# Kernel tuning notes

Hardware: AMD Instinct MI355X
Metric: run time of the kernel (lower is better)

Reference implementation:

```python
import jax, jax.numpy as jnp
import numpy as np

NQ, NT, BSZ, E, NH = 100, 197, 128, 768, 12
HD = E // NH
EPS = 1e-12  # torch F.normalize default eps


def _l2norm(x, axis=-1):
    n = jnp.linalg.norm(x, axis=axis, keepdims=True)
    return x / jnp.maximum(n, EPS)


def setup_inputs() -> dict:
    rng = jax.random.key(0)
    ks = jax.random.split(rng, 10)
    s = 0.02  # xavier-ish scale for weights
    return {
        "query": jax.random.normal(ks[0], (NQ, BSZ, E), jnp.float32),
        "key": jax.random.normal(ks[1], (NT, BSZ, E), jnp.float32),
        "value": jax.random.normal(ks[2], (NT, BSZ, E), jnp.float32),
        "in_proj_weight": jax.random.normal(ks[3], (3 * E, E), jnp.float32) * s,
        "in_proj_bias": jnp.zeros((3 * E,), jnp.float32),
        "out_proj_weight": jax.random.normal(ks[4], (E, E), jnp.float32) * s,
        "out_proj_bias": jnp.zeros((E,), jnp.float32),
        "temperature": jnp.ones((NH, 1, 1), jnp.float32),
        "q_mapper": jax.random.normal(ks[5], (1, NT, NQ), jnp.float32),
        "x_mapper": jax.random.normal(ks[6], (1, NQ, NT), jnp.float32),
    }


def reference(query, key, value, in_proj_weight, in_proj_bias,
              out_proj_weight, out_proj_bias, temperature, q_mapper, x_mapper):
    nq, bsz, e = query.shape
    nt = key.shape[0]
    # packed in-projection: split into q/k/v weights
    wq, wk, wv = jnp.split(in_proj_weight, 3, axis=0)
    bq, bk, bv = jnp.split(in_proj_bias, 3, axis=0)
    q = query @ wq.T + bq   # [Nq, bsz, E]
    k = key @ wk.T + bk     # [Nt, bsz, E]
    v = value @ wv.T + bv   # [Nt, bsz, E]
    # reshape to [bsz, nh, hd, N] (channel-major for cross-covariance attn)
    q = q.reshape(nq, bsz, NH, HD).transpose(1, 2, 3, 0)  # [b, h, d, Nq]
    k = k.reshape(nt, bsz, NH, HD).transpose(1, 2, 3, 0)  # [b, h, d, Nt]
    v = v.reshape(nt, bsz, NH, HD).transpose(1, 2, 3, 0)  # [b, h, d, Nt]
    # normalize channel vectors over tokens
    qn = _l2norm(q)
    kn = _l2norm(k)
    # mappers: normalize over last dim, then shape to [Nq, Nt] operators
    qm_op = _l2norm(q_mapper[0])  # [Nt, Nq] normalized over Nq; transpose below
    xm_op = _l2norm(x_mapper[0])  # [Nq, Nt] normalized over Nt
    # qm = q @ q_mapper^T : [b,h,d,Nq] x [Nq,Nt] -> [b,h,d,Nt]
    qm = jnp.einsum('bhdq,tq->bhdt', qn, qm_op)
    # cross-covariance attention over channels: [b,h,d,d]
    attn = jnp.einsum('bhdt,bhet->bhde', qm, kn) * temperature[None]  # temp [nh,1,1] broadcasts per-head
    attn = jax.nn.softmax(attn, axis=-1)
    x = jnp.einsum('bhde,bhet->bhdt', attn, v)        # [b,h,d,Nt]
    out = jnp.einsum('bhdt,qt->bhdq', x, xm_op)       # [b,h,d,Nq]
    # back to [Nq, bsz, E]
    out = out.transpose(3, 0, 1, 2).reshape(nq, bsz, e)
    out = out @ out_proj_weight.T + out_proj_bias
    return out
```

## Files before the change

kernel.cpp:

```cpp
#include <hip/hip_runtime.h>
#include <hip/hip_bf16.h>

using bf16 = __hip_bfloat16;

constexpr int NQ  = 100;
constexpr int NT  = 197;
constexpr int BSZ = 128;
constexpr int EMB = 768;
constexpr int NHD = 12;
constexpr int HDD = 64;
constexpr int COLS = BSZ * EMB;
constexpr int M_Q  = 12800;
constexpr int M_KV = 25216;
constexpr int M_KVP = 25344;
constexpr int TPAD = 224;

constexpr size_t SZ_Q16  = (size_t)M_Q  * EMB * 2;
constexpr size_t SZ_KV16 = (size_t)M_KV * EMB * 2;
constexpr size_t SZ_KVP  = (size_t)M_KVP * EMB * 2;
constexpr size_t SZ_WI   = (size_t)3 * EMB * EMB * 2;
constexpr size_t SZ_T16  = (size_t)COLS * TPAD * 2;
constexpr size_t OFF_QB   = 256;
constexpr size_t OFF_KB   = OFF_QB + SZ_Q16;
constexpr size_t OFF_VB   = OFF_KB + SZ_KV16;
constexpr size_t OFF_WI   = OFF_VB + SZ_KV16;
constexpr size_t OFF_QP16 = OFF_WI + SZ_WI;
constexpr size_t OFF_KP16 = OFF_QP16 + SZ_Q16;
constexpr size_t OFF_VP16 = OFF_KP16 + SZ_KVP;
constexpr size_t OFF_QMNT = OFF_VP16 + SZ_KVP;
constexpr size_t OFF_XMNT = OFF_QMNT + 57344;
constexpr size_t OFF_WO   = OFF_XMNT + 57344;
constexpr size_t OFF_KPT  = 256;
constexpr size_t OFF_VPT  = OFF_KPT + SZ_T16;
constexpr size_t OFF_W16T = OFF_VPT + SZ_T16;
constexpr size_t OFF_QNT  = OFF_KP16;
constexpr size_t OFF_G16  = OFF_VP16;
constexpr size_t OFF_XO   = 256;

__device__ __forceinline__ float dl(const float* p) { return *p; }
__device__ __forceinline__ float dl(const bf16* p) { return __bfloat162float(*p); }

__device__ __forceinline__ ushort f2bf(float x) {
    union { float f; unsigned u; } v; v.f = x;
    unsigned r = v.u + 0x7FFFu + ((v.u >> 16) & 1u);
    return (ushort)(r >> 16);
}
__device__ __forceinline__ float bf2f(ushort x) {
    union { unsigned u; float f; } v; v.u = (unsigned)x << 16;
    return v.f;
}
__device__ __forceinline__ void dstore(float* p, float v) { *p = v; }
__device__ __forceinline__ void dstore(bf16* p, float v) { *p = __float2bfloat16(v); }

typedef __attribute__((ext_vector_type(8))) short short8;
typedef __attribute__((ext_vector_type(4))) short shortv4;
typedef __attribute__((ext_vector_type(4))) float f32x4;

__device__ __forceinline__ void gload16(const bf16* g, ushort* l) {
    __builtin_amdgcn_global_load_lds(
        (const __attribute__((address_space(1))) unsigned int*)g,
        (__attribute__((address_space(3))) unsigned int*)l, 16, 0, 0);
}

__device__ __forceinline__ int2 xcd_swz(int bx, int by, int gx, int gy) {
    const int nwg = gx * gy;
    const int L = by * gx + bx;
    const int q = nwg >> 3, r = nwg & 7;
    const int c = L & 7, i = L >> 3;
    const int wg = (c < r ? c * (q + 1) : r * (q + 1) + (c - r) * q) + i;
    return make_int2(wg % gx, wg / gx);
}

template <typename TM>
__global__ __launch_bounds__(256) void k_cvt5(
        const float* __restrict__ s0, bf16* __restrict__ d0,
        const float* __restrict__ s1, bf16* __restrict__ d1,
        const float* __restrict__ s2, bf16* __restrict__ d2,
        const float* __restrict__ s3, bf16* __restrict__ d3,
        const float* __restrict__ s4, bf16* __restrict__ d4,
        const TM* __restrict__ qm, bf16* __restrict__ qmnT,
        const TM* __restrict__ xm, bf16* __restrict__ xmnT) {
    int bk = blockIdx.x;
    const int tid = threadIdx.x;
    if (bk >= 24864) {
        __shared__ float red[256];
        if (bk < 25088) {
            int t = bk - 24864;
            float v = (t < NT && tid < NQ) ? dl(&qm[t * NQ + tid]) : 0.f;
            if (tid < 128) red[tid] = v * v;
            __syncthreads();
            for (int s = 64; s > 0; s >>= 1) { if (tid < s) red[tid] += red[tid + s]; __syncthreads(); }
            float inv = 1.f / fmaxf(sqrtf(red[0]), 1e-12f);
            if (tid < 128)
                dstore(&qmnT[(size_t)tid * TPAD + t], (t < NT && tid < NQ) ? v * inv : 0.f);
        } else {
            int q = bk - 25088, t = tid;
            float v = (q < NQ && t < NT) ? dl(&xm[q * NT + t]) : 0.f;
            red[t] = v * v;
            __syncthreads();
            for (int s = 128; s > 0; s >>= 1) { if (t < s) red[t] += red[t + s]; __syncthreads(); }
            float inv = 1.f / fmaxf(sqrtf(red[0]), 1e-12f);
            if (t < TPAD) dstore(&xmnT[(size_t)q * TPAD + t], (q < NQ && t < NT) ? v * inv : 0.f);
        }
        return;
    }
    const float* s; bf16* d; int lb;
    if      (bk < 864)   { s = s0; d = d0; lb = bk; }
    else if (bk < 5664)  { s = s1; d = d1; lb = bk - 864; }
    else if (bk < 15120) { s = s2; d = d2; lb = bk - 5664; }
    else if (bk < 24576) { s = s3; d = d3; lb = bk - 15120; }
    else                 { s = s4; d = d4; lb = bk - 24576; }
    size_t i = ((size_t)lb * 256 + tid) * 8;
    float4 a = *(const float4*)(s + i), b = *(const float4*)(s + i + 4);
    short8 r;
    r[0] = (short)f2bf(a.x); r[1] = (short)f2bf(a.y); r[2] = (short)f2bf(a.z); r[3] = (short)f2bf(a.w);
    r[4] = (short)f2bf(b.x); r[5] = (short)f2bf(b.y); r[6] = (short)f2bf(b.z); r[7] = (short)f2bf(b.w);
    *(short8*)(d + i) = r;
}

template <typename T>
__global__ __launch_bounds__(256) void k_maps(const T* __restrict__ qm, bf16* qmnT,
                                              const T* __restrict__ xm, bf16* xmnT) {
    __shared__ float red[256];
    const int bk = blockIdx.x, tid = threadIdx.x;
    if (bk < 224) {
        int t = bk;
        float v = (t < NT && tid < NQ) ? dl(&qm[t * NQ + tid]) : 0.f;
        if (tid < 128) red[tid] = v * v;
        __syncthreads();
        for (int s = 64; s > 0; s >>= 1) { if (tid < s) red[tid] += red[tid + s]; __syncthreads(); }
        float inv = 1.f / fmaxf(sqrtf(red[0]), 1e-12f);
        if (tid < 128)
            dstore(&qmnT[(size_t)tid * TPAD + t], (t < NT && tid < NQ) ? v * inv : 0.f);
    } else {
        int q = bk - 224, t = tid;
        float v = (q < NQ && t < NT) ? dl(&xm[q * NT + t]) : 0.f;
        red[t] = v * v;
        __syncthreads();
        for (int s = 128; s > 0; s >>= 1) { if (t < s) red[t] += red[t + s]; __syncthreads(); }
        float inv = 1.f / fmaxf(sqrtf(red[0]), 1e-12f);
        if (t < TPAD) dstore(&xmnT[(size_t)q * TPAD + t], (q < NQ && t < NT) ? v * inv : 0.f);
    }
}

template <int NR, int TP, int NORM>
__global__ __launch_bounds__(256) void k_trn(const bf16* __restrict__ src,
        bf16* __restrict__ dst) {
    __shared__ ushort tile[TP * 73];
    __shared__ float ssp[4][64];
    __shared__ float inv_s[64];
    const int col0 = blockIdx.x * 64;
    const int tid = threadIdx.x;
    const int c = tid & 63, tb = tid >> 6;
    float ss = 0.f;
#pragma unroll
    for (int it = 0; it < TP / 4; ++it) {
        int t = tb + it * 4;
        ushort v = 0;
        if (t < NR) v = *(const ushort*)&src[(size_t)t * COLS + col0 + c];
        tile[t * 73 + c] = v;
        if (NORM) { float f = bf2f(v); ss = fmaf(f, f, ss); }
    }
    if (NORM) {
        ssp[tb][c] = ss;
        __syncthreads();
        if (tid < 64) {
            float s = ssp[0][tid] + ssp[1][tid] + ssp[2][tid] + ssp[3][tid];
            inv_s[tid] = 1.f / fmaxf(sqrtf(s), 1e-12f);
        }
    }
    __syncthreads();
    constexpr int UPC = TP / 8;
#pragma unroll
    for (int it = 0; it < (64 * UPC) / 256; ++it) {
        int u = tid + it * 256;
        int cc = u / UPC, t0 = (u % UPC) * 8;
        float inv = NORM ? inv_s[cc] : 1.f;
        short8 s;
#pragma unroll
        for (int r = 0; r < 8; ++r) {
            ushort raw = tile[(t0 + r) * 73 + cc];
            s[r] = NORM ? (short)f2bf(bf2f(raw) * inv) : (short)raw;
        }
        *(short8*)&dst[(size_t)(col0 + cc) * TP + t0] = s;
    }
}

__global__ __launch_bounds__(256) void k_trn2(const bf16* __restrict__ kp,
        const bf16* __restrict__ vp, bf16* __restrict__ kpT, bf16* __restrict__ vpT) {
    __shared__ ushort tile[TPAD * 73];
    __shared__ float ssp[4][64];
    __shared__ float inv_s[64];
    const int bk = blockIdx.x;
    const bool vseg = bk >= 1536;
    const bf16* src = vseg ? vp : kp;
    bf16* dst = vseg ? vpT : kpT;
    const int col0 = (vseg ? bk - 1536 : bk) * 64;
    const int tid = threadIdx.x;
    const int c = tid & 63, tb = tid >> 6;
    float ss = 0.f;
#pragma unroll
    for (int it = 0; it < TPAD / 4; ++it) {
        int t = tb + it * 4;
        ushort v = 0;
        if (t < NT) v = *(const ushort*)&src[(size_t)t * COLS + col0 + c];
        tile[t * 73 + c] = v;
        if (!vseg) { float f = bf2f(v); ss = fmaf(f, f, ss); }
    }
    if (!vseg) {
        ssp[tb][c] = ss;
        __syncthreads();
        if (tid < 64) {
            float s = ssp[0][tid] + ssp[1][tid] + ssp[2][tid] + ssp[3][tid];
            inv_s[tid] = 1.f / fmaxf(sqrtf(s), 1e-12f);
        }
    }
    __syncthreads();
    constexpr int UPC = TPAD / 8;
#pragma unroll
    for (int it = 0; it < (64 * UPC) / 256; ++it) {
        int u = tid + it * 256;
        int cc = u / UPC, t0 = (u % UPC) * 8;
        float inv = vseg ? 1.f : inv_s[cc];
        short8 s;
#pragma unroll
        for (int r = 0; r < 8; ++r) {
            ushort raw = tile[(t0 + r) * 73 + cc];
            s[r] = vseg ? (short)raw : (short)f2bf(bf2f(raw) * inv);
        }
        *(short8*)&dst[(size_t)(col0 + cc) * TPAD + t0] = s;
    }
}

#define MM8_BAR  { __builtin_amdgcn_s_barrier(); __builtin_amdgcn_sched_barrier(0); }
#define MM8_LGK0 { asm volatile("s_waitcnt lgkmcnt(0)" ::: "memory"); __builtin_amdgcn_sched_barrier(0); }
#define MM8_VM8  { asm volatile("s_waitcnt vmcnt(8)" ::: "memory"); __builtin_amdgcn_sched_barrier(0); }
#define MM8_VM0  { asm volatile("s_waitcnt vmcnt(0)" ::: "memory"); __builtin_amdgcn_sched_barrier(0); }
#define MM8_STAGE(CUR, ISB, H, KT) do { \
    const bf16* gb_ = (ISB) ? (Wb + (size_t)(n0 + (H)*128 + srow) * EMB + (KT)*64 + sk_sw) \
                            : (Ab + (size_t)(m0 + (H)*128 + srow) * EMB + (KT)*64 + sk_sw); \
    ushort* lb_ = ((ISB) ? B_lds : A_lds) + (CUR)*16384 + (H)*8192 + wid*512; \
    gload16(gb_, lb_); \
    gload16(gb_ + (size_t)64 * EMB, lb_ + 4096); \
} while (0)
#define MM8_LOADFRAGS(CUR, KK, AARR, BARR) { \
    _Pragma("unroll") for (int m_ = 0; m_ < 8; ++m_) { \
        int ra_ = wr*128 + m_*16 + ln15; \
        AARR[m_] = *(const short8*)&A_lds[(CUR)*16384 + ra_*64 + ((((KK)*4 + q8) ^ (ra_ & 7)))*8]; } \
    _Pragma("unroll") for (int j_ = 0; j_ < 4; ++j_) { \
        int rb_ = wc*64 + j_*16 + ln15; \
        BARR[j_] = *(const short8*)&B_lds[(CUR)*16384 + rb_*64 + ((((KK)*4 + q8) ^ (rb_ & 7)))*8]; } }
#define MM8_QUAD(AARR, BARR, MB) { \
    __builtin_amdgcn_s_setprio(1); \
    _Pragma("unroll") for (int m_ = 0; m_ < 4; ++m_) \
        _Pragma("unroll") for (int j_ = 0; j_ < 4; ++j_) \
            acc[(MB) + m_][j_] = __builtin_amdgcn_mfma_f32_16x16x32_bf16( \
                AARR[(MB) + m_], BARR[j_], acc[(MB) + m_][j_], 0, 0, 0); \
    __builtin_amdgcn_s_setprio(0); }

template <typename TC>
__global__ __launch_bounds__(512, 2) void k_mm8(
        const bf16* __restrict__ A0, const bf16* __restrict__ A1, const bf16* __restrict__ A2,
        const bf16* __restrict__ W,
        TC* __restrict__ C0, TC* __restrict__ C1, TC* __restrict__ C2,
        const float* __restrict__ bias, int mt0, int mt01) {
    __shared__ __align__(16) ushort A_lds[2 * 16384];
    __shared__ __align__(16) ushort B_lds[2 * 16384];
    const int tid = threadIdx.x;
    const int2 bxy = xcd_swz(blockIdx.x, blockIdx.y, gridDim.x, gridDim.y);
    int seg = 0, lby = bxy.y;
    if (bxy.y < mt0)       { seg = 0; lby = bxy.y; }
    else if (bxy.y < mt01) { seg = 1; lby = bxy.y - mt0; }
    else                   { seg = 2; lby = bxy.y - mt01; }
    const bf16* Ab = seg == 0 ? A0 : (seg == 1 ? A1 : A2);
    const bf16* Wb = W + (size_t)seg * EMB * EMB;
    TC* C = seg == 0 ? C0 : (seg == 1 ? C1 : C2);
    const float* bp = bias + seg * EMB;
    const int m0 = lby * 256, n0 = bxy.x * 256;
    const int wid = tid >> 6, ln = tid & 63;
    const int wr = wid >> 2, wc = wid & 3;
    const int ln15 = ln & 15, q8 = ln >> 4;
    const int srow = tid >> 3;
    const int sk_sw = (((tid & 7) ^ (srow & 7)) * 8);

    f32x4 acc[8][4] = {};
    short8 a0[8], b0[4], a1[8], b1[4];

    MM8_STAGE(0, 0, 0, 0); MM8_STAGE(0, 0, 1, 0); MM8_STAGE(0, 1, 0, 0); MM8_STAGE(0, 1, 1, 0);
    MM8_STAGE(1, 0, 0, 1); MM8_STAGE(1, 0, 1, 1); MM8_STAGE(1, 1, 0, 1); MM8_STAGE(1, 1, 1, 1);
    MM8_VM8;
    MM8_BAR;

    for (int t = 0; t < 12; ++t) {
        const int c = t & 1, nxt = t + 2;
        MM8_LOADFRAGS(c, 0, a0, b0);
        MM8_QUAD(a0, b0, 0);
        MM8_LOADFRAGS(c, 1, a1, b1);
        MM8_QUAD(a0, b0, 4);
        MM8_LGK0;
        MM8_BAR;
        if (nxt < 12) { MM8_STAGE(c, 0, 0, nxt); MM8_STAGE(c, 0, 1, nxt); }
        MM8_QUAD(a1, b1, 0);
        if (nxt < 12) { MM8_STAGE(c, 1, 0, nxt); MM8_STAGE(c, 1, 1, nxt); }
        if (t < 10) { MM8_VM8; } else { MM8_VM0; }
        MM8_QUAD(a1, b1, 4);
        MM8_BAR;
    }

#pragma unroll
    for (int j = 0; j < 4; ++j) {
        const int n = n0 + wc * 64 + j * 16 + ln15;
        const float bv = bp[n];
#pragma unroll
        for (int m = 0; m < 8; ++m) {
            const int mb = m0 + wr * 128 + m * 16 + q8 * 4;
#pragma unroll
            for (int r = 0; r < 4; ++r)
                dstore(&C[(size_t)(mb + r) * EMB + n], acc[m][j][r] + bv);
        }
    }
}

template <typename TBias>
__global__ __launch_bounds__(256) void k_proj2(
        const bf16* __restrict__ Aq, const bf16* __restrict__ Ak, const bf16* __restrict__ Av,
        const bf16* __restrict__ Wi, bf16* __restrict__ Cq, bf16* __restrict__ Ck,
        bf16* __restrict__ Cv, const TBias* __restrict__ bias) {
    __shared__ __align__(16) ushort As[128 * 32];
    __shared__ __align__(16) ushort Bs[128 * 32];
    const int t = threadIdx.x;
    const int2 bxy = xcd_swz(blockIdx.x, blockIdx.y, gridDim.x, gridDim.y);
    int byy = bxy.y, seg, lby;
    if (byy < 100)      { seg = 0; lby = byy; }
    else if (byy < 297) { seg = 1; lby = byy - 100; }
    else                { seg = 2; lby = byy - 297; }
    const bf16* Ab = seg == 0 ? Aq : (seg == 1 ? Ak : Av);
    const bf16* Wb = Wi + (size_t)seg * EMB * EMB;
    bf16* C = seg == 0 ? Cq : (seg == 1 ? Ck : Cv);
    const TBias* bp = bias + seg * EMB;
    const int n0 = bxy.x * 128, m0 = lby * 128;
    const int ln = t & 63, wv = t >> 6;
    const int ln15 = ln & 15, q8 = ln >> 4;
    const int mw = (wv & 1) * 64, nw = (wv >> 1) * 64;
    const int sr = ln >> 2, sk = (ln & 3) * 8;
    const bf16* gA = Ab + (size_t)(m0 + wv * 32 + sr) * EMB + sk;
    const bf16* gB = Wb + (size_t)(n0 + wv * 32 + sr) * EMB + sk;
    const size_t r16 = (size_t)16 * EMB;
    ushort* lA = &As[wv * 1024];
    ushort* lB = &Bs[wv * 1024];
    f32x4 acc[4][4] = {};
    for (int k0 = 0; k0 < EMB; k0 += 32) {
        gload16(gA + k0,       lA);
        gload16(gA + r16 + k0, lA + 512);
        gload16(gB + k0,       lB);
        gload16(gB + r16 + k0, lB + 512);
        __syncthreads();
        short8 a[4], b[4];
#pragma unroll
        for (int i = 0; i < 4; ++i)
            a[i] = *(const short8*)&As[(mw + i * 16 + ln15) * 32 + q8 * 8];
#pragma unroll
        for (int j = 0; j < 4; ++j)
            b[j] = *(const short8*)&Bs[(nw + j * 16 + ln15) * 32 + q8 * 8];
#pragma unroll
        for (int i = 0; i < 4; ++i)
#pragma unroll
            for (int j = 0; j < 4; ++j)
                acc[i][j] = __builtin_amdgcn_mfma_f32_16x16x32_bf16(a[i], b[j], acc[i][j], 0, 0, 0);
        __syncthreads();
    }
#pragma unroll
    for (int j = 0; j < 4; ++j) {
        const int n = n0 + nw + j * 16 + ln15;
        const float bv = dl(&bp[n]);
#pragma unroll
        for (int i = 0; i < 4; ++i) {
            const int mb = m0 + mw + i * 16 + q8 * 4;
#pragma unroll
            for (int r = 0; r < 4; ++r)
                dstore(&C[(size_t)(mb + r) * EMB + n], acc[i][j][r] + bv);
        }
    }
}

__global__ __launch_bounds__(256) void k_gw(
        const bf16* __restrict__ kpT, const bf16* __restrict__ vpT,
        const bf16* __restrict__ qmnT, const bf16* __restrict__ xmnT,
        bf16* __restrict__ g16, bf16* __restrict__ w16T) {
    __shared__ __align__(16) ushort As[128 * 32];
    __shared__ __align__(16) ushort Bs[128 * 32];
    const int t = threadIdx.x;
    const int2 bxy = xcd_swz(blockIdx.x, blockIdx.y, gridDim.x, gridDim.y);
    const bool wseg = bxy.y >= 768;
    const int lby = wseg ? bxy.y - 768 : bxy.y;
    const bf16* Ab = wseg ? vpT : kpT;
    const bf16* Bb = wseg ? xmnT : qmnT;
    const int m0 = lby * 128;
    const int ln = t & 63, wv = t >> 6;
    const int ln15 = ln & 15, q8 = ln >> 4;
    const int mw = (wv & 1) * 64, nw = (wv >> 1) * 64;
    const int sr = ln >> 2, sk = (ln & 3) * 8;
    const bf16* gA = Ab + (size_t)(m0 + wv * 32 + sr) * TPAD + sk;
    const bf16* gB = Bb + (size_t)(wv * 32 + sr) * TPAD + sk;
    const size_t r16 = (size_t)16 * TPAD;
    ushort* lA = &As[wv * 1024];
    ushort* lB = &Bs[wv * 1024];
    f32x4 acc[4][4] = {};
    for (int k0 = 0; k0 < TPAD; k0 += 32) {
        gload16(gA + k0,       lA);
        gload16(gA + r16 + k0, lA + 512);
        gload16(gB + k0,       lB);
        gload16(gB + r16 + k0, lB + 512);
        __syncthreads();
        short8 a[4], b[4];
#pragma unroll
        for (int i = 0; i < 4; ++i)
            a[i] = *(const short8*)&As[(mw + i * 16 + ln15) * 32 + q8 * 8];
#pragma unroll
        for (int j = 0; j < 4; ++j)
            b[j] = *(const short8*)&Bs[(nw + j * 16 + ln15) * 32 + q8 * 8];
#pragma unroll
        for (int i = 0; i < 4; ++i)
#pragma unroll
            for (int j = 0; j < 4; ++j)
                acc[i][j] = __builtin_amdgcn_mfma_f32_16x16x32_bf16(a[i], b[j], acc[i][j], 0, 0, 0);
        __syncthreads();
    }
#pragma unroll
    for (int j = 0; j < 4; ++j) {
        const int n = nw + j * 16 + ln15;
#pragma unroll
        for (int i = 0; i < 4; ++i) {
            const int mb = m0 + mw + i * 16 + q8 * 4;
            if (wseg) {
                shortv4 s;
#pragma unroll
                for (int r = 0; r < 4; ++r) s[r] = (short)f2bf(acc[i][j][r]);
                *(shortv4*)&w16T[(size_t)n * COLS + mb] = s;
            } else {
#pragma unroll
                for (int r = 0; r < 4; ++r)
                    dstore(&g16[(size_t)(mb + r) * 128 + n], acc[i][j][r]);
            }
        }
    }
}

template <typename TC, typename TBias>
__global__ __launch_bounds__(256) void k_gemm_mfma(
        const bf16* __restrict__ Ab, const bf16* __restrict__ Wb,
        TC* __restrict__ C, const TBias* __restrict__ bias,
        int M, int N, int K, int ldc) {
    __shared__ __align__(16) ushort As[128 * 32];
    __shared__ __align__(16) ushort Bs[128 * 32];
    const int t = threadIdx.x;
    const int2 bxy = xcd_swz(blockIdx.x, blockIdx.y, gridDim.x, gridDim.y);
    const int n0 = bxy.x * 128, m0 = bxy.y * 128;
    const int ln = t & 63, wv = t >> 6;
    const int ln15 = ln & 15, q8 = ln >> 4;
    const int mw = (wv & 1) * 64, nw = (wv >> 1) * 64;
    const int sr = ln >> 2, sk = (ln & 3) * 8;
    const bf16* gA = Ab + (size_t)(m0 + wv * 32 + sr) * K + sk;
    const bf16* gB = Wb + (size_t)(n0 + wv * 32 + sr) * K + sk;
    const size_t r16 = (size_t)16 * K;
    ushort* lA = &As[wv * 1024];
    ushort* lB = &Bs[wv * 1024];
    f32x4 acc[4][4] = {};
    for (int k0 = 0; k0 < K; k0 += 32) {
        gload16(gA + k0,       lA);
        gload16(gA + r16 + k0, lA + 512);
        gload16(gB + k0,       lB);
        gload16(gB + r16 + k0, lB + 512);
        __syncthreads();
        short8 a[4], b[4];
#pragma unroll
        for (int i = 0; i < 4; ++i)
            a[i] = *(const short8*)&As[(mw + i * 16 + ln15) * 32 + q8 * 8];
#pragma unroll
        for (int j = 0; j < 4; ++j)
            b[j] = *(const short8*)&Bs[(nw + j * 16 + ln15) * 32 + q8 * 8];
#pragma unroll
        for (int i = 0; i < 4; ++i)
#pragma unroll
            for (int j = 0; j < 4; ++j)
                acc[i][j] = __builtin_amdgcn_mfma_f32_16x16x32_bf16(a[i], b[j], acc[i][j], 0, 0, 0);
        __syncthreads();
    }
#pragma unroll
    for (int j = 0; j < 4; ++j) {
        const int n = n0 + nw + j * 16 + ln15;
        const float bv = dl(&bias[n]);
#pragma unroll
        for (int i = 0; i < 4; ++i) {
            const int mb = m0 + mw + i * 16 + q8 * 4;
#pragma unroll
            for (int r = 0; r < 4; ++r)
                dstore(&C[(size_t)(mb + r) * ldc + n], acc[i][j][r] + bv);
        }
    }
}

template <typename T>
__global__ __launch_bounds__(256) void k_attn(
        const bf16* __restrict__ qnT, const bf16* __restrict__ g16,
        const bf16* __restrict__ w16T, const T* __restrict__ temp,
        bf16* __restrict__ xo) {
    const int h = blockIdx.x, b = blockIdx.y;
    const int tid = threadIdx.x;
    const int ln = tid & 63, wv = tid >> 6;
    const int ln15 = ln & 15, q8 = ln >> 4;
    const int colbase = b * EMB + h * HDD;
    __shared__ __align__(16) ushort smem[16384];
    char* sm = (char*)smem;

    short8 wreg[4];
#pragma unroll
    for (int it = 0; it < 4; ++it) {
        int u = tid + it * 256;
        int q = u >> 3, e0 = (u & 7) * 8;
        wreg[it] = *(const short8*)&w16T[(size_t)q * COLS + colbase + e0];
    }

#pragma unroll
    for (int it = 0; it < 4; ++it) {
        int u = tid + it * 256;
        int e = u >> 4, q0 = (u & 15) * 8;
        short8 s = *(const short8*)&g16[(size_t)(colbase + e) * 128 + q0];
        *(short8*)(sm + ((e * 256 + q0 * 2) ^ ((e & 7) << 4))) = s;
    }
#pragma unroll
    for (int it = 0; it < 4; ++it) {
        int u = tid + it * 256;
        int d = u >> 4, q0 = (u & 15) * 8;
        short8 s = *(const short8*)&qnT[(size_t)(colbase + d) * 128 + q0];
        *(short8*)(sm + 16384 + ((d * 256 + q0 * 2) ^ ((d & 7) << 4))) = s;
    }
    __syncthreads();

    const int drow = 16 * wv + ln15;
    f32x4 acc[4] = {};
#pragma unroll
    for (int ks = 0; ks < 4; ++ks) {
        short8 bfrag = *(const short8*)(sm + 16384 +
            ((drow * 256 + ks * 64 + q8 * 16) ^ ((drow & 7) << 4)));
#pragma unroll
        for (int i = 0; i < 4; ++i) {
            int erow = i * 16 + ln15;
            short8 afrag = *(const short8*)(sm +
                ((erow * 256 + ks * 64 + q8 * 16) ^ ((erow & 7) << 4)));
            acc[i] = __builtin_amdgcn_mfma_f32_16x16x32_bf16(afrag, bfrag, acc[i], 0, 0, 0);
        }
    }

    const float tv = dl(&temp[h]);
    float p[4][4];
    float mx = -1e30f;
#pragma unroll
    for (int i = 0; i < 4; ++i)
#pragma unroll
        for (int r = 0; r < 4; ++r) { p[i][r] = acc[i][r] * tv; mx = fmaxf(mx, p[i][r]); }
    mx = fmaxf(mx, __shfl_xor(mx, 16, 64));
    mx = fmaxf(mx, __shfl_xor(mx, 32, 64));
    float sum = 0.f;
#pragma unroll
    for (int i = 0; i < 4; ++i)
#pragma unroll
        for (int r = 0; r < 4; ++r) { p[i][r] = __expf(p[i][r] - mx); sum += p[i][r]; }
    sum += __shfl_xor(sum, 16, 64);
    sum += __shfl_xor(sum, 32, 64);
    const float rs = 1.f / sum;

    __syncthreads();

#pragma unroll
    for (int i = 0; i < 4; ++i) {
        shortv4 s4;
#pragma unroll
        for (int r = 0; r < 4; ++r) s4[r] = (short)f2bf(p[i][r] * rs);
        *(shortv4*)(sm + 16384 + drow * 144 + q8 * 8 + 32 * i) = s4;
    }
#pragma unroll
    for (int it = 0; it < 4; ++it) {
        int u = tid + it * 256;
        int q = u >> 3, e0 = (u & 7) * 8;
        *(short8*)(sm + ((q * 128 + e0 * 2) ^ ((q & 7) << 4))) = wreg[it];
    }
    __syncthreads();

    f32x4 o[7] = {};
#pragma unroll
    for (int ks = 0; ks < 2; ++ks) {
        short8 afrag = *(const short8*)(sm + 16384 + drow * 144 + ks * 64 + q8 * 16);
#pragma unroll
        for (int j = 0; j < 7; ++j) {
            int qrow = j * 16 + ln15;
            short8 bfrag = *(const short8*)(sm +
                ((qrow * 128 + ks * 64 + q8 * 16) ^ ((qrow & 7) << 4)));
            o[j] = __builtin_amdgcn_mfma_f32_16x16x32_bf16(afrag, bfrag, o[j], 0, 0, 0);
        }
    }
    const int dbase = h * HDD + 16 * wv + q8 * 4;
#pragma unroll
    for (int j = 0; j < 7; ++j) {
        int q = j * 16 + ln15;
        if (q < NQ) {
            shortv4 s4;
#pragma unroll
            for (int r = 0; r < 4; ++r) s4[r] = (short)f2bf(o[j][r]);
            *(shortv4*)&xo[(size_t)(q * BSZ + b) * EMB + dbase] = s4;
        }
    }
}

extern "C" void kernel_launch(void* const* d_in, const int* in_sizes, int n_in,
                              void* d_out, int out_size, void* d_ws, size_t ws_size,
                              hipStream_t stream) {
    char* ws = (char*)d_ws;
    bf16* qb16  = (bf16*)(ws + OFF_QB);
    bf16* kb16  = (bf16*)(ws + OFF_KB);
    bf16* vb16  = (bf16*)(ws + OFF_VB);
    bf16* wi16  = (bf16*)(ws + OFF_WI);
    bf16* qp16  = (bf16*)(ws + OFF_QP16);
    bf16* kp16  = (bf16*)(ws + OFF_KP16);
    bf16* vp16  = (bf16*)(ws + OFF_VP16);
    bf16* qmnT  = (bf16*)(ws + OFF_QMNT);
    bf16* xmnT  = (bf16*)(ws + OFF_XMNT);
    bf16* wo16  = (bf16*)(ws + OFF_WO);
    bf16* kpT   = (bf16*)(ws + OFF_KPT);
    bf16* vpT   = (bf16*)(ws + OFF_VPT);
    bf16* w16T  = (bf16*)(ws + OFF_W16T);
    bf16* qnT   = (bf16*)(ws + OFF_QNT);
    bf16* g16   = (bf16*)(ws + OFF_G16);
    bf16* xo16  = (bf16*)(ws + OFF_XO);

    const bool isbf = (in_sizes[0] == 19660800);

    if (isbf) {
        k_maps<bf16><<<352, 256, 0, stream>>>((const bf16*)d_in[8], qmnT,
                                              (const bf16*)d_in[9], xmnT);
        k_proj2<bf16><<<dim3(6, 494), 256, 0, stream>>>(
            (const bf16*)d_in[0], (const bf16*)d_in[1], (const bf16*)d_in[2],
            (const bf16*)d_in[3], qp16, kp16, vp16, (const bf16*)d_in[4]);
        k_trn2<<<3072, 256, 0, stream>>>(kp16, vp16, kpT, vpT);
        k_trn<NQ, 128, 1><<<COLS / 64, 256, 0, stream>>>(qp16, qnT);
        k_gw<<<dim3(1, 1536), 256, 0, stream>>>(kpT, vpT, qmnT, xmnT, g16, w16T);
        k_attn<bf16><<<dim3(NHD, BSZ), 256, 0, stream>>>(
            qnT, g16, w16T, (const bf16*)d_in[7], xo16);
        k_gemm_mfma<bf16, bf16><<<dim3(6, 100), 256, 0, stream>>>(
            xo16, (const bf16*)d_in[5], (bf16*)d_out, (const bf16*)d_in[6],
            M_Q, EMB, EMB, EMB);
    } else {
        k_cvt5<float><<<25216, 256, 0, stream>>>(
            (const float*)d_in[3], wi16,
            (const float*)d_in[0], qb16,
            (const float*)d_in[1], kb16,
            (const float*)d_in[2], vb16,
            (const float*)d_in[5], wo16,
            (const float*)d_in[8], qmnT,
            (const float*)d_in[9], xmnT);
        k_mm8<bf16><<<dim3(3, 248), 512, 0, stream>>>(
            qb16, kb16, vb16, wi16, qp16, kp16, vp16,
            (const float*)d_in[4], 50, 149);
        k_trn2<<<3072, 256, 0, stream>>>(kp16, vp16, kpT, vpT);
        k_trn<NQ, 128, 1><<<COLS / 64, 256, 0, stream>>>(qp16, qnT);
        k_gw<<<dim3(1, 1536), 256, 0, stream>>>(kpT, vpT, qmnT, xmnT, g16, w16T);
        k_attn<float><<<dim3(NHD, BSZ), 256, 0, stream>>>(
            qnT, g16, w16T, (const float*)d_in[7], xo16);
        k_mm8<float><<<dim3(3, 50), 512, 0, stream>>>(
            xo16, nullptr, nullptr, wo16, (float*)d_out, nullptr, nullptr,
            (const float*)d_in[6], 50, 50);
    }
}
```

Measured before the change: 451.0 us.

## Fuse fp32-to-bf16 activation conversion into the QKV projection GEMM

The separate conversion pass that turned the fp32 query/key/value activations into bf16 buffers is removed. A new GEMM kernel loads the fp32 activations straight into LDS and converts them to bf16 while building MFMA fragments, with a K-step of 32 per stage. The conversion kernel now only handles the weights and the mapper normalisation. This drops a full read and write of about 150MB of activations, in exchange for twice the LDS bandwidth per A element, more K iterations, and conversion ALU work inside the GEMM main loop.

```diff
diff --git a/kernel.cpp b/kernel.cpp
--- a/kernel.cpp
+++ b/kernel.cpp
@@ -61,6 +61,11 @@
         (const __attribute__((address_space(1))) unsigned int*)g,
         (__attribute__((address_space(3))) unsigned int*)l, 16, 0, 0);
 }
+__device__ __forceinline__ void gload16f(const float* g, ushort* l) {
+    __builtin_amdgcn_global_load_lds(
+        (const __attribute__((address_space(1))) unsigned int*)g,
+        (__attribute__((address_space(3))) unsigned int*)l, 16, 0, 0);
+}
 
 __device__ __forceinline__ int2 xcd_swz(int bx, int by, int gx, int gy) {
     const int nwg = gx * gy;
@@ -71,51 +76,43 @@
     return make_int2(wg % gx, wg / gx);
 }
 
-template <typename TM>
-__global__ __launch_bounds__(256) void k_cvt5(
-        const float* __restrict__ s0, bf16* __restrict__ d0,
-        const float* __restrict__ s1, bf16* __restrict__ d1,
-        const float* __restrict__ s2, bf16* __restrict__ d2,
-        const float* __restrict__ s3, bf16* __restrict__ d3,
-        const float* __restrict__ s4, bf16* __restrict__ d4,
-        const TM* __restrict__ qm, bf16* __restrict__ qmnT,
-        const TM* __restrict__ xm, bf16* __restrict__ xmnT) {
-    int bk = blockIdx.x;
-    const int tid = threadIdx.x;
-    if (bk >= 24864) {
-        __shared__ float red[256];
-        if (bk < 25088) {
-            int t = bk - 24864;
-            float v = (t < NT && tid < NQ) ? dl(&qm[t * NQ + tid]) : 0.f;
-            if (tid < 128) red[tid] = v * v;
-            __syncthreads();
-            for (int s = 64; s > 0; s >>= 1) { if (tid < s) red[tid] += red[tid + s]; __syncthreads(); }
-            float inv = 1.f / fmaxf(sqrtf(red[0]), 1e-12f);
-            if (tid < 128)
-                dstore(&qmnT[(size_t)tid * TPAD + t], (t < NT && tid < NQ) ? v * inv : 0.f);
-        } else {
-            int q = bk - 25088, t = tid;
-            float v = (q < NQ && t < NT) ? dl(&xm[q * NT + t]) : 0.f;
-            red[t] = v * v;
-            __syncthreads();
-            for (int s = 128; s > 0; s >>= 1) { if (t < s) red[t] += red[t + s]; __syncthreads(); }
-            float inv = 1.f / fmaxf(sqrtf(red[0]), 1e-12f);
-            if (t < TPAD) dstore(&xmnT[(size_t)q * TPAD + t], (q < NQ && t < NT) ? v * inv : 0.f);
-        }
+__global__ __launch_bounds__(256) void k_cvtw(
+        const float* __restrict__ swi, bf16* __restrict__ dwi,
+        const float* __restrict__ swo, bf16* __restrict__ dwo,
+        const float* __restrict__ qm, bf16* __restrict__ qmnT,
+        const float* __restrict__ xm, bf16* __restrict__ xmnT) {
+    const int bk = blockIdx.x, tid = threadIdx.x;
+    if (bk < 1152) {
+        const float* s = bk < 864 ? swi : swo;
+        bf16* d = bk < 864 ? dwi : dwo;
+        int lb = bk < 864 ? bk : bk - 864;
+        size_t i = ((size_t)lb * 256 + tid) * 8;
+        float4 a = *(const float4*)(s + i), b = *(const float4*)(s + i + 4);
+        short8 r;
+        r[0] = (short)f2bf(a.x); r[1] = (short)f2bf(a.y); r[2] = (short)f2bf(a.z); r[3] = (short)f2bf(a.w);
+        r[4] = (short)f2bf(b.x); r[5] = (short)f2bf(b.y); r[6] = (short)f2bf(b.z); r[7] = (short)f2bf(b.w);
+        *(short8*)(d + i) = r;
         return;
     }
-    const float* s; bf16* d; int lb;
-    if      (bk < 864)   { s = s0; d = d0; lb = bk; }
-    else if (bk < 5664)  { s = s1; d = d1; lb = bk - 864; }
-    else if (bk < 15120) { s = s2; d = d2; lb = bk - 5664; }
-    else if (bk < 24576) { s = s3; d = d3; lb = bk - 15120; }
-    else                 { s = s4; d = d4; lb = bk - 24576; }
-    size_t i = ((size_t)lb * 256 + tid) * 8;
-    float4 a = *(const float4*)(s + i), b = *(const float4*)(s + i + 4);
-    short8 r;
-    r[0] = (short)f2bf(a.x); r[1] = (short)f2bf(a.y); r[2] = (short)f2bf(a.z); r[3] = (short)f2bf(a.w);
-    r[4] = (short)f2bf(b.x); r[5] = (short)f2bf(b.y); r[6] = (short)f2bf(b.z); r[7] = (short)f2bf(b.w);
-    *(short8*)(d + i) = r;
+    __shared__ float red[256];
+    if (bk < 1376) {
+        int t = bk - 1152;
+        float v = (t < NT && tid < NQ) ? qm[t * NQ + tid] : 0.f;
+        if (tid < 128) red[tid] = v * v;
+        __syncthreads();
+        for (int s = 64; s > 0; s >>= 1) { if (tid < s) red[tid] += red[tid + s]; __syncthreads(); }
+        float inv = 1.f / fmaxf(sqrtf(red[0]), 1e-12f);
+        if (tid < 128)
+            dstore(&qmnT[(size_t)tid * TPAD + t], (t < NT && tid < NQ) ? v * inv : 0.f);
+    } else {
+        int q = bk - 1376, t = tid;
+        float v = (q < NQ && t < NT) ? xm[q * NT + t] : 0.f;
+        red[t] = v * v;
+        __syncthreads();
+        for (int s = 128; s > 0; s >>= 1) { if (t < s) red[t] += red[t + s]; __syncthreads(); }
+        float inv = 1.f / fmaxf(sqrtf(red[0]), 1e-12f);
+        if (t < TPAD) dstore(&xmnT[(size_t)q * TPAD + t], (q < NQ && t < NT) ? v * inv : 0.f);
+    }
 }
 
 template <typename T>
@@ -229,6 +226,108 @@
             s[r] = vseg ? (short)raw : (short)f2bf(bf2f(raw) * inv);
         }
         *(short8*)&dst[(size_t)(col0 + cc) * TPAD + t0] = s;
+    }
+}
+
+#define MMF_BAR  { __builtin_amdgcn_s_barrier(); __builtin_amdgcn_sched_barrier(0); }
+#define MMF_LGK0 { asm volatile("s_waitcnt lgkmcnt(0)" ::: "memory"); __builtin_amdgcn_sched_barrier(0); }
+#define MMF_VM8  { asm volatile("s_waitcnt vmcnt(8)" ::: "memory"); __builtin_amdgcn_sched_barrier(0); }
+#define MMF_VM0  { asm volatile("s_waitcnt vmcnt(0)" ::: "memory"); __builtin_amdgcn_sched_barrier(0); }
+#define MMF_STAGE_A(CUR, G, KT) do { \
+    int rr_ = m0 + (G)*64 + (tid >> 3); if (rr_ >= mrows) rr_ = mrows - 1; \
+    const float* ga_ = Af + (size_t)rr_ * EMB + (KT)*32 + skA; \
+    gload16f(ga_, A_lds + (CUR)*16384 + (G)*4096 + tid*8); \
+} while (0)
+#define MMF_STAGE_B(CUR, G, KT) do { \
+    int rr_ = n0 + (G)*64 + (tid >> 3); \
+    const bf16* gb_ = Wb + (size_t)rr_ * EMB + (KT)*32 + skB; \
+    gload16(gb_, B_lds + (CUR)*16384 + (G)*4096 + tid*8); \
+} while (0)
+#define MMF_LOADFRAGS(CUR, AARR, BARR) { \
+    _Pragma("unroll") for (int m_ = 0; m_ < 8; ++m_) { \
+        int ra_ = wr*128 + m_*16 + ln15; \
+        int ab_ = (CUR)*16384 + ra_*64; \
+        f32x4 f0_ = *(const f32x4*)&A_lds[ab_ + (((2*q8) ^ (ra_ & 7)))*8]; \
+        f32x4 f1_ = *(const f32x4*)&A_lds[ab_ + (((2*q8 + 1) ^ (ra_ & 7)))*8]; \
+        short8 t_; \
+        t_[0]=(short)f2bf(f0_[0]); t_[1]=(short)f2bf(f0_[1]); t_[2]=(short)f2bf(f0_[2]); t_[3]=(short)f2bf(f0_[3]); \
+        t_[4]=(short)f2bf(f1_[0]); t_[5]=(short)f2bf(f1_[1]); t_[6]=(short)f2bf(f1_[2]); t_[7]=(short)f2bf(f1_[3]); \
+        AARR[m_] = t_; } \
+    _Pragma("unroll") for (int j_ = 0; j_ < 4; ++j_) { \
+        int rb_ = wc*64 + j_*16 + ln15; \
+        BARR[j_] = *(const short8*)&B_lds[(CUR)*16384 + rb_*64 + ((q8 ^ (rb_ & 7)))*8]; } }
+#define MMF_QUAD(AARR, BARR, MB) { \
+    __builtin_amdgcn_s_setprio(1); \
+    _Pragma("unroll") for (int m_ = 0; m_ < 4; ++m_) \
+        _Pragma("unroll") for (int j_ = 0; j_ < 4; ++j_) \
+            acc[(MB) + m_][j_] = __builtin_amdgcn_mfma_f32_16x16x32_bf16( \
+                AARR[(MB) + m_], BARR[j_], acc[(MB) + m_][j_], 0, 0, 0); \
+    __builtin_amdgcn_s_setprio(0); }
+
+__global__ __launch_bounds__(512, 2) void k_mm8f(
+        const float* __restrict__ A0, const float* __restrict__ A1, const float* __restrict__ A2,
+        const bf16* __restrict__ W,
+        bf16* __restrict__ C0, bf16* __restrict__ C1, bf16* __restrict__ C2,
+        const float* __restrict__ bias, int mt0, int mt01) {
+    __shared__ __align__(16) ushort A_lds[2 * 16384];
+    __shared__ __align__(16) ushort B_lds[2 * 16384];
+    const int tid = threadIdx.x;
+    const int2 bxy = xcd_swz(blockIdx.x, blockIdx.y, gridDim.x, gridDim.y);
+    int seg = 0, lby = bxy.y;
+    if (bxy.y < mt0)       { seg = 0; lby = bxy.y; }
+    else if (bxy.y < mt01) { seg = 1; lby = bxy.y - mt0; }
+    else                   { seg = 2; lby = bxy.y - mt01; }
+    const float* Af = seg == 0 ? A0 : (seg == 1 ? A1 : A2);
+    const bf16* Wb = W + (size_t)seg * EMB * EMB;
+    bf16* C = seg == 0 ? C0 : (seg == 1 ? C1 : C2);
+    const float* bp = bias + seg * EMB;
+    const int mrows = seg == 0 ? M_Q : M_KV;
+    const int m0 = lby * 256, n0 = bxy.x * 256;
+    const int wid = tid >> 6, ln = tid & 63;
+    const int wr = wid >> 2, wc = wid & 3;
+    const int ln15 = ln & 15, q8 = ln >> 4;
+    const int lsw = (tid & 7) ^ ((tid >> 3) & 7);
+    const int skA = lsw * 4;
+    const int skB = (lsw & 3) * 8;
+
+    f32x4 acc[8][4] = {};
+    short8 a0[8], b0[4];
+
+    MMF_STAGE_A(0, 0, 0); MMF_STAGE_A(0, 1, 0); MMF_STAGE_A(0, 2, 0); MMF_STAGE_A(0, 3, 0);
+    MMF_STAGE_B(0, 0, 0); MMF_STAGE_B(0, 1, 0); MMF_STAGE_B(0, 2, 0); MMF_STAGE_B(0, 3, 0);
+    MMF_STAGE_A(1, 0, 1); MMF_STAGE_A(1, 1, 1); MMF_STAGE_A(1, 2, 1); MMF_STAGE_A(1, 3, 1);
+    MMF_STAGE_B(1, 0, 1); MMF_STAGE_B(1, 1, 1); MMF_STAGE_B(1, 2, 1); MMF_STAGE_B(1, 3, 1);
+    MMF_VM8;
+    MMF_BAR;
+
+    for (int t = 0; t < 24; ++t) {
+        const int c = t & 1, nxt = t + 2;
+        MMF_LOADFRAGS(c, a0, b0);
+        MMF_QUAD(a0, b0, 0);
+        MMF_LGK0;
+        MMF_BAR;
+        if (nxt < 24) {
+            MMF_STAGE_A(c, 0, nxt); MMF_STAGE_A(c, 1, nxt);
+            MMF_STAGE_A(c, 2, nxt); MMF_STAGE_A(c, 3, nxt);
+            MMF_STAGE_B(c, 0, nxt); MMF_STAGE_B(c, 1, nxt);
+            MMF_STAGE_B(c, 2, nxt); MMF_STAGE_B(c, 3, nxt);
+        }
+        if (t < 22) { MMF_VM8; } else { MMF_VM0; }
+        MMF_QUAD(a0, b0, 4);
+        MMF_BAR;
+    }
+
+#pragma unroll
+    for (int j = 0; j < 4; ++j) {
+        const int n = n0 + wc * 64 + j * 16 + ln15;
+        const float bv = bp[n];
+#pragma unroll
+        for (int m = 0; m < 8; ++m) {
+            const int mb = m0 + wr * 128 + m * 16 + q8 * 4;
+#pragma unroll
+            for (int r = 0; r < 4; ++r)
+                dstore(&C[(size_t)(mb + r) * EMB + n], acc[m][j][r] + bv);
+        }
     }
 }
 
@@ -616,9 +715,6 @@
                               void* d_out, int out_size, void* d_ws, size_t ws_size,
                               hipStream_t stream) {
     char* ws = (char*)d_ws;
-    bf16* qb16  = (bf16*)(ws + OFF_QB);
-    bf16* kb16  = (bf16*)(ws + OFF_KB);
-    bf16* vb16  = (bf16*)(ws + OFF_VB);
     bf16* wi16  = (bf16*)(ws + OFF_WI);
     bf16* qp16  = (bf16*)(ws + OFF_QP16);
     bf16* kp16  = (bf16*)(ws + OFF_KP16);
@@ -650,17 +746,14 @@
             xo16, (const bf16*)d_in[5], (bf16*)d_out, (const bf16*)d_in[6],
             M_Q, EMB, EMB, EMB);
     } else {
-        k_cvt5<float><<<25216, 256, 0, stream>>>(
+        k_cvtw<<<1504, 256, 0, stream>>>(
             (const float*)d_in[3], wi16,
-            (const float*)d_in[0], qb16,
-            (const float*)d_in[1], kb16,
-            (const float*)d_in[2], vb16,
             (const float*)d_in[5], wo16,
             (const float*)d_in[8], qmnT,
             (const float*)d_in[9], xmnT);
-        k_mm8<bf16><<<dim3(3, 248), 512, 0, stream>>>(
-            qb16, kb16, vb16, wi16, qp16, kp16, vp16,
-            (const float*)d_in[4], 50, 149);
+        k_mm8f<<<dim3(3, 248), 512, 0, stream>>>(
+            (const float*)d_in[0], (const float*)d_in[1], (const float*)d_in[2],
+            wi16, qp16, kp16, vp16, (const float*)d_in[4], 50, 149);
         k_trn2<<<3072, 256, 0, stream>>>(kp16, vp16, kpT, vpT);
         k_trn<NQ, 128, 1><<<COLS / 64, 256, 0, stream>>>(qp16, qnT);
         k_gw<<<dim3(1, 1536), 256, 0, stream>>>(kpT, vpT, qmnT, xmnT, g16, w16T);
```

Result: slower. 479.2 us (+6.2%).
